# Kernel tuning notes

Measured on AMD Instinct MI355X. Metric: run time of the kernel, lower is better.

Reference implementation:

```python
import jax, jax.numpy as jnp
from jax import lax
import numpy as np

B, K, H, W = 16, 8, 256, 256


def setup_inputs() -> dict:
    key = jax.random.key(0)
    masks = jax.random.normal(key, (B, K, H, W), dtype=jnp.float32)
    return {"masks": masks}


def _nlccs_loss_one(mask):
    """Per-mask loss. mask: (H, W) float, already rescaled/clamped.

    Replicates cv2.connectedComponentsWithStats (8-connectivity, background is
    a single label regardless of connectivity), sorts components by area, and
    suppresses (zeroes a pmask over) the bounding box of the second-largest
    component, then returns mean(pmask * mask).
    """
    h, w = mask.shape
    S = h * w  # sentinel / background label
    sent = jnp.int32(S)
    fg = lax.stop_gradient(mask) > 0.5  # cv2 threshold (arr > 0.5)
    idx = jnp.arange(S, dtype=jnp.int32).reshape(h, w)
    lab0 = jnp.where(fg, idx, sent)

    def step(lab):
        # 8-connectivity neighbor-min propagation (cv2 default connectivity=8)
        p = jnp.pad(lab, 1, constant_values=S)
        m = lab
        for dy in (-1, 0, 1):
            for dx in (-1, 0, 1):
                if dy == 0 and dx == 0:
                    continue
                m = jnp.minimum(m, p[1 + dy:1 + dy + h, 1 + dx:1 + dx + w])
        lab = jnp.where(fg, m, sent)
        # pointer jumping: lab <- lab[lab] for log-time convergence
        ext = jnp.concatenate([lab.reshape(-1), jnp.array([S], jnp.int32)])
        return jnp.where(fg, ext[lab], sent)

    def cond(c):
        lab, prev = c
        return jnp.any(lab != prev)

    def body(c):
        lab, _ = c
        return step(lab), lab

    lab, _ = lax.while_loop(cond, body, (step(lab0), lab0))

    # per-label areas; background pixels all share label S (like cv2 label 0)
    areas = jnp.zeros(S + 1, jnp.int32).at[lab.reshape(-1)].add(1)
    _, top_idx = lax.top_k(areas, 2)
    second = top_idx[1]  # stats sorted by area -> stats[-2]

    # bounding box of the second-largest component
    sel = lab == second
    rows = jnp.arange(h, dtype=jnp.int32)[:, None]
    cols = jnp.arange(w, dtype=jnp.int32)[None, :]
    h0 = jnp.min(jnp.where(sel, rows, h))
    h1 = jnp.max(jnp.where(sel, rows, -1)) + 1
    w0 = jnp.min(jnp.where(sel, cols, w))
    w1 = jnp.max(jnp.where(sel, cols, -1)) + 1
    inside = (rows >= h0) & (rows < h1) & (cols >= w0) & (cols < w1)
    pmask = 1.0 - inside.astype(mask.dtype)  # pmask[h0:h1, w0:w1] = 0
    return (pmask * mask).mean()


def reference(masks):
    # masks: (b, k, h, w)
    m = jnp.maximum((masks + 1.0) * 0.5, 0.0)  # ((masks+1)/2).clamp(min=0)
    flat = m.reshape(-1, m.shape[-2], m.shape[-1])  # (b*k, h, w)
    losses = jax.vmap(_nlccs_loss_one)(flat)
    return losses.mean()
```

## Files before the change

kernel.cpp:

```cpp
#include <hip/hip_runtime.h>

#define HH 256
#define WW 256
#define SS 65536
#define NM 128
#define TRR 16
#define NT2 16
#define RMX 2048
#define SPT 1024
#define SPM 16384

struct Meta {
  double dsum[NM];
  int h0[NM]; int h1[NM]; int w0[NM]; int w1[NM];
};

__device__ __forceinline__ int find_c(int* L, int x) {
  int p = L[x];
  if (p == x) return x;
  int root = p, q = L[root];
  while (q != root) { root = q; q = L[root]; }
  if (root != p) L[x] = root;
  return root;
}

__device__ void unite(int* L, int a, int b) {
  bool done = false;
  do {
    a = find_c(L, a);
    b = find_c(L, b);
    if (a < b)      { int old = atomicMin(&L[b], a); done = (old == b); b = old; }
    else if (b < a) { int old = atomicMin(&L[a], b); done = (old == a); a = old; }
    else done = true;
  } while (!done);
}

__device__ __forceinline__ int find_halve(int* L, int x) {
  int p = L[x];
  while (p != x) {
    int gp = L[p];
    if (gp == p) return p;
    L[x] = gp;
    x = p; p = gp;
  }
  return x;
}

__device__ __forceinline__ int cid(const unsigned long long* rm,
                                   const int* rpre, int r) {
  int w = r >> 6, b = r & 63;
  return rpre[w] + (int)__popcll(rm[w] & (b ? ((1ull << b) - 1) : 0ull));
}

__device__ __forceinline__ unsigned long long mask_le(int b) {
  return (b == 63) ? ~0ull : ((1ull << (b + 1)) - 1);
}
__device__ __forceinline__ unsigned long long mask_lt(int b) {
  return b ? ((1ull << b) - 1) : 0ull;
}

__global__ __launch_bounds__(512)
void k_local(const float* __restrict__ in, int cb,
             int* __restrict__ gp, int* __restrict__ ga,
             unsigned int* __restrict__ gbb, unsigned short* __restrict__ gl,
             unsigned short* __restrict__ gbrow, int* __restrict__ gnr,
             double* __restrict__ tdsum, unsigned int* __restrict__ tbb,
             int* __restrict__ gfg0) {
  __shared__ unsigned long long sfgw[TRR][4];
  __shared__ unsigned char sfgc[TRR][32];
  __shared__ unsigned long long srs[TRR][4];
  __shared__ int wpre64[64];
  __shared__ int snr;
  __shared__ int sspan[RMX];
  __shared__ int suf[RMX];
  __shared__ unsigned long long rootm[32];
  __shared__ int rpre[32];
  __shared__ int sA[SPT], sW0[SPT], sW1[SPT], sH0[SPT], sH1[SPT];
  __shared__ double sred[8];
  __shared__ int sbb[4][8];

  int q = blockIdx.x, lm = q >> 4, tile = q & 15;
  int tid = threadIdx.x, lane = tid & 63, wv = tid >> 6;
  int gm = cb + lm, R0 = tile << 4;

  int r1 = tid >> 5, cs = tid & 31;
  const float4* src =
      (const float4*)(in + ((size_t)gm << 16) + ((R0 + r1) << 8) + (cs << 3));
  double dsum = 0.0;
  unsigned int fgb = 0;
  for (int k = 0; k < 2; k++) {
    float4 v = src[k];
    float m0 = fmaxf((v.x + 1.0f) * 0.5f, 0.0f);
    float m1 = fmaxf((v.y + 1.0f) * 0.5f, 0.0f);
    float m2 = fmaxf((v.z + 1.0f) * 0.5f, 0.0f);
    float m3 = fmaxf((v.w + 1.0f) * 0.5f, 0.0f);
    dsum += (double)m0 + (double)m1 + (double)m2 + (double)m3;
    fgb |= ((m0 > 0.5f) ? 1u : 0u) << (4 * k);
    fgb |= ((m1 > 0.5f) ? 1u : 0u) << (4 * k + 1);
    fgb |= ((m2 > 0.5f) ? 1u : 0u) << (4 * k + 2);
    fgb |= ((m3 > 0.5f) ? 1u : 0u) << (4 * k + 3);
  }
  sfgc[r1][cs] = (unsigned char)fgb;
  __syncthreads();
  if (tid < 64) {
    int row = tid >> 2, w = tid & 3;
    const unsigned char* pc = &sfgc[row][w << 3];
    unsigned long long wd = 0;
    for (int i = 0; i < 8; i++) wd |= ((unsigned long long)pc[i]) << (i << 3);
    sfgw[row][w] = wd;
  }
  __syncthreads();

  if (tid < 64) {
    int row = tid >> 2, w = tid & 3;
    unsigned long long W = sfgw[row][w];
    unsigned long long carry = (w > 0) ? (sfgw[row][w - 1] >> 63) : 0ull;
    unsigned long long rs = W & ~((W << 1) | carry);
    srs[row][w] = rs;
    int cnt = (int)__popcll(rs);
    int sa = cnt;
    for (int off = 1; off < 64; off <<= 1) {
      int t = __shfl_up(sa, off);
      if (tid >= off) sa += t;
    }
    wpre64[tid] = sa - cnt;
    if (tid == 63) snr = sa;
    int id = sa - cnt;
    unsigned long long bits = rs;
    while (bits) {
      int a = (int)__ffsll(bits) - 1;
      bits &= bits - 1;
      int A = (w << 6) + a;
      unsigned long long inv = ~(W >> a);
      int len = inv ? ((int)__ffsll(inv) - 1) : (64 - a);
      if (len == 64 - a) {
        for (int w2 = w + 1; w2 < 4; w2++) {
          unsigned long long iv2 = ~sfgw[row][w2];
          int t = iv2 ? ((int)__ffsll(iv2) - 1) : 64;
          len += t;
          if (t < 64) break;
        }
      }
      sspan[id] = (row << 16) | (A << 8) | (A + len - 1);
      suf[id] = id;
      id++;
    }
  } else {
    for (int s = tid - 64; s < SPT; s += 448) {
      sA[s] = 0; sW0[s] = WW; sW1[s] = -1; sH0[s] = TRR; sH1[s] = -1;
    }
  }
  __syncthreads();

  int nr = snr;

  for (int i = tid; i < nr; i += 512) {
    int sp = sspan[i];
    int row = sp >> 16, a = (sp >> 8) & 255, b = sp & 255;
    if (row == 0) continue;
    int lo = max(a - 1, 0), hi = min(b + 1, 255);
    const unsigned long long* Wp = sfgw[row - 1];
    const unsigned long long* Rp = srs[row - 1];
    int prebase = (row - 1) << 2;
    int lw = lo >> 6, lb = lo & 63;
    if (((Wp[lw] >> lb) & 1) && !((Rp[lw] >> lb) & 1)) {
      int j = wpre64[prebase + lw] + (int)__popcll(Rp[lw] & mask_le(lb)) - 1;
      unite(suf, i, j);
    }
    for (int w = lw; w <= (hi >> 6); w++) {
      unsigned long long m = Rp[w];
      if (w == lw) m &= ~mask_lt(lb);
      if (w == (hi >> 6)) m &= mask_le(hi & 63);
      int base2 = wpre64[prebase + w];
      while (m) {
        int bb = (int)__ffsll(m) - 1;
        m &= m - 1;
        int j = base2 + (int)__popcll(Rp[w] & mask_lt(bb));
        unite(suf, i, j);
      }
    }
  }
  __syncthreads();

  for (int j = 0; j < 4; j++) {
    int i = tid + (j << 9);
    unsigned long long bal = __ballot(i < nr && suf[i] == i);
    if (lane == 0) rootm[wv + (j << 3)] = bal;
  }
  __syncthreads();
  if (tid < 32) {
    int pc = (int)__popcll(rootm[tid]);
    int sa = pc;
    for (int off = 1; off < 32; off <<= 1) {
      int t = __shfl_up(sa, off);
      if (tid >= off) sa += t;
    }
    rpre[tid] = sa - pc;
  }
  __syncthreads();

  for (int i = tid; i < nr; i += 512) {
    int root = find_halve(suf, i);
    int id = cid(rootm, rpre, root);
    int sp = sspan[i];
    int row = sp >> 16, a = (sp >> 8) & 255, b = sp & 255;
    atomicAdd(&sA[id], b - a + 1);
    if (a < sW0[id]) atomicMin(&sW0[id], a);
    if (b > sW1[id]) atomicMax(&sW1[id], b);
    if (row < sH0[id]) atomicMin(&sH0[id], row);
    if (row > sH1[id]) atomicMax(&sH1[id], row);
  }
  __syncthreads();

  int nc = rpre[31] + (int)__popcll(rootm[31]);
  for (int i = tid; i < nr; i += 512) {
    if (suf[i] == i) {
      int id = cid(rootm, rpre, i);
      int gid = (lm << 14) + (tile << 10) + id;
      int sp = sspan[i];
      gp[gid] = gid;
      ga[gid] = sA[id];
      gl[gid] = (unsigned short)((tile << 12) + ((sp >> 16) << 8) +
                                 ((sp >> 8) & 255));
      gbb[gid] = ((unsigned)(R0 + sH0[id]) << 24) | ((unsigned)sW0[id] << 16)
               | ((unsigned)(R0 + sH1[id]) << 8) | (unsigned)sW1[id];
    }
  }
  {
    int c = tid & 255, topbot = tid >> 8;
    int brow = topbot ? (TRR - 1) : 0;
    unsigned short val = 0xFFFF;
    if ((sfgw[brow][c >> 6] >> (c & 63)) & 1) {
      int w = c >> 6, bb = c & 63;
      int id = wpre64[(brow << 2) + w] +
               (int)__popcll(srs[brow][w] & mask_le(bb)) - 1;
      int root = find_halve(suf, id);
      val = (unsigned short)((tile << 10) + cid(rootm, rpre, root));
    }
    gbrow[(q << 9) + (topbot ? 256 : 0) + c] = val;
  }
  if (tid == 0) gnr[q] = nc;

  int c = tid & 255, half = (tid >> 8) << 3;
  int bh0r = TRR, bh1r = -1;
  bool anybg = false;
  for (int row = half; row < half + 8; row++) {
    if (!((sfgw[row][c >> 6] >> (c & 63)) & 1)) {
      anybg = true;
      bh0r = min(bh0r, row); bh1r = max(bh1r, row);
    }
  }
  int bw0r = anybg ? c : WW, bw1r = anybg ? c : -1;
  for (int off = 32; off > 0; off >>= 1) {
    bw0r = min(bw0r, __shfl_down(bw0r, off));
    bw1r = max(bw1r, __shfl_down(bw1r, off));
    bh0r = min(bh0r, __shfl_down(bh0r, off));
    bh1r = max(bh1r, __shfl_down(bh1r, off));
  }
  if (lane == 0) { sbb[0][wv] = bw0r; sbb[1][wv] = bw1r;
                   sbb[2][wv] = bh0r; sbb[3][wv] = bh1r; }
  for (int off = 32; off > 0; off >>= 1) dsum += __shfl_down(dsum, off);
  if (lane == 0) sred[wv] = dsum;
  __syncthreads();
  if (tid == 0) {
    int a0 = sbb[0][0], a1 = sbb[1][0], a2 = sbb[2][0], a3 = sbb[3][0];
    for (int i = 1; i < 8; i++) {
      a0 = min(a0, sbb[0][i]); a1 = max(a1, sbb[1][i]);
      a2 = min(a2, sbb[2][i]); a3 = max(a3, sbb[3][i]);
    }
    unsigned pack = (a1 >= 0)
        ? (((unsigned)(R0 + a2) << 24) | ((unsigned)a0 << 16) |
           ((unsigned)(R0 + a3) << 8) | (unsigned)a1)
        : 0xFFFF0000u;
    tbb[q] = pack;
    double t = 0.0;
    for (int i = 0; i < 8; i++) t += sred[i];
    tdsum[q] = t;
    if (tile == 0) gfg0[lm] = (int)(sfgw[0][0] & 1ull);
  }
}

__global__ void k_seam(int* __restrict__ gp,
                       const unsigned short* __restrict__ gbrow) {
  int b = blockIdx.x;
  int lm = b / 15, s = b % 15;
  int tb = lm << 4;
  int sbase = lm << 14;
  const unsigned short* up = gbrow + ((tb + s) << 9) + 256;
  const unsigned short* lo = gbrow + ((tb + s + 1) << 9);
  int c = threadIdx.x;
  unsigned short v16 = lo[c];
  if (v16 == 0xFFFF) return;
  int v = sbase + v16;
  bool wfg = (c > 0) && (lo[c - 1] != 0xFFFF);
  unsigned short n16 = up[c];
  if (!wfg) {
    if (n16 != 0xFFFF) unite(gp, v, sbase + n16);
    else if (c > 0 && up[c - 1] != 0xFFFF) unite(gp, v, sbase + up[c - 1]);
  }
  if (n16 == 0xFFFF && c < 255 && up[c + 1] != 0xFFFF)
    unite(gp, v, sbase + up[c + 1]);
}

__global__ void k_push(int* __restrict__ gp, int* __restrict__ ga,
                       const int* __restrict__ gnr) {
  int q = blockIdx.x;
  int lm = q >> 4;
  int sbase = lm << 14;
  int nc = gnr[q];
  int tid = threadIdx.x, lane = tid & 63;
  for (int t = 0; t < 4; t++) {
    int slot = (t << 8) + tid;
    int r = -1, a = 0;
    if (slot < nc) {
      int gid = sbase + ((q & 15) << 10) + slot;
      int rr = find_c(gp, gid);
      if (rr != gid) { r = rr; a = ga[gid]; }
    }
    bool pend = (r >= 0);
    while (__any(pend)) {
      unsigned long long mk = __ballot(pend);
      int srcl = (int)__ffsll(mk) - 1;
      int lead = __shfl(r, srcl);
      bool mine = pend && (r == lead);
      int v = mine ? a : 0;
      for (int off = 32; off > 0; off >>= 1) v += __shfl_down(v, off);
      int tot = __shfl(v, 0);
      if (lane == srcl) atomicAdd(&ga[lead], tot);
      pend = pend && !mine;
    }
  }
}

__global__ __launch_bounds__(1024)
void k_mask(int* __restrict__ gp, const int* __restrict__ ga,
            const unsigned int* __restrict__ gbb,
            const unsigned short* __restrict__ gl,
            const int* __restrict__ gnr,
            const double* __restrict__ tdsum,
            const unsigned int* __restrict__ tbb,
            const int* __restrict__ gfg0,
            Meta* __restrict__ mt, int c0) {
  int lm = blockIdx.x, gm = c0 + lm;
  int tid = threadIdx.x;
  int tb = lm << 4;
  int sbase = lm << 14;
  int wv = tid >> 6, lane = tid & 63;
  __shared__ int sbg[4];
  __shared__ int snr16[16];

  if (tid >= 64 && tid < 80) snr16[tid - 64] = gnr[tb + (tid - 64)];
  if (tid < 64) {
    double d = 0.0;
    int h0 = 255, w0 = 255, h1 = 0, w1 = 0;
    if (tid < 16) {
      d = tdsum[tb + tid];
      unsigned bb = tbb[tb + tid];
      h0 = (int)(bb >> 24); w0 = (int)((bb >> 16) & 255);
      h1 = (int)((bb >> 8) & 255); w1 = (int)(bb & 255);
    }
    for (int off = 8; off > 0; off >>= 1) {
      d += __shfl_down(d, off);
      h0 = min(h0, __shfl_down(h0, off));
      w0 = min(w0, __shfl_down(w0, off));
      h1 = max(h1, __shfl_down(h1, off));
      w1 = max(w1, __shfl_down(w1, off));
    }
    if (tid == 0) {
      mt->dsum[gm] = d;
      sbg[0] = h0; sbg[1] = h1; sbg[2] = w0; sbg[3] = w1;
    }
  }
  __syncthreads();

  unsigned long long t1 = 0, t2 = 0;
  int fsum = 0;
  for (int s = tid; s < SPM; s += 1024) {
    if ((s & (SPT - 1)) >= snr16[s >> 10]) continue;
    int gid = sbase + s;
    if (gp[gid] == gid) {
      int a = ga[gid];
      int lab = gl[gid];
      fsum += a;
      unsigned long long key = ((unsigned long long)a << 37)
                             | ((unsigned long long)(SS - lab) << 20)
                             | (unsigned)s;
      if (key > t1) { t2 = t1; t1 = key; }
      else if (key > t2) t2 = key;
    }
  }
  for (int off = 32; off > 0; off >>= 1) {
    unsigned long long o1 = __shfl_down(t1, off), o2 = __shfl_down(t2, off);
    if (o1 > t1) { t2 = (t1 > o2) ? t1 : o2; t1 = o1; }
    else if (o1 > t2) t2 = o1;
    fsum += __shfl_down(fsum, off);
  }
  __shared__ unsigned long long s1[16], s2[16];
  __shared__ int sf[16];
  __shared__ int ssel, sslot;
  if (lane == 0) { s1[wv] = t1; s2[wv] = t2; sf[wv] = fsum; }
  __syncthreads();
  if (tid == 0) {
    t1 = s1[0]; t2 = s2[0]; fsum = sf[0];
    for (int i = 1; i < 16; i++) {
      unsigned long long o1 = s1[i], o2 = s2[i];
      if (o1 > t1) { t2 = (t1 > o2) ? t1 : o2; t1 = o1; }
      else if (o1 > t2) t2 = o1;
      fsum += sf[i];
    }
    unsigned long long bg = ((unsigned long long)(SS - fsum)) << 37;
    int zl = gfg0[lm] ? 1 : 0;
    unsigned long long zk = ((unsigned long long)(SS - zl)) << 20;
    if (bg > t1) { t2 = t1; t1 = bg; } else if (bg > t2) t2 = bg;
    if (zk > t1) { t2 = t1; t1 = zk; } else if (zk > t2) t2 = zk;
    if (t2 == bg) {
      ssel = 1;
      mt->h0[gm] = sbg[0]; mt->h1[gm] = sbg[1];
      mt->w0[gm] = sbg[2]; mt->w1[gm] = sbg[3];
    } else if (t2 == zk) {
      ssel = 2;
      mt->h0[gm] = 1; mt->h1[gm] = 0; mt->w0[gm] = 1; mt->w1[gm] = 0;
    } else {
      ssel = 0; sslot = (int)(t2 & 0xFFFFF);
    }
  }
  __syncthreads();

  if (ssel == 0) {
    int secgid = sbase + sslot;
    int h0l = HH, h1l = -1, w0l = WW, w1l = -1;
    for (int s = tid; s < SPM; s += 1024) {
      if ((s & (SPT - 1)) >= snr16[s >> 10]) continue;
      int i = sbase + s;
      if (find_c(gp, i) == secgid) {
        unsigned int bb = gbb[i];
        h0l = min(h0l, (int)(bb >> 24));
        w0l = min(w0l, (int)((bb >> 16) & 255));
        h1l = max(h1l, (int)((bb >> 8) & 255));
        w1l = max(w1l, (int)(bb & 255));
      }
    }
    for (int off = 32; off > 0; off >>= 1) {
      h0l = min(h0l, __shfl_down(h0l, off));
      w0l = min(w0l, __shfl_down(w0l, off));
      h1l = max(h1l, __shfl_down(h1l, off));
      w1l = max(w1l, __shfl_down(w1l, off));
    }
    __shared__ int r0[16], r1[16], r2[16], r3[16];
    if (lane == 0) { r0[wv] = h0l; r1[wv] = h1l; r2[wv] = w0l; r3[wv] = w1l; }
    __syncthreads();
    if (tid == 0) {
      for (int i = 1; i < 16; i++) {
        r0[0] = min(r0[0], r0[i]); r1[0] = max(r1[0], r1[i]);
        r2[0] = min(r2[0], r2[i]); r3[0] = max(r3[0], r3[i]);
      }
      mt->h0[gm] = r0[0]; mt->h1[gm] = r1[0];
      mt->w0[gm] = r2[0]; mt->w1[gm] = r3[0];
    }
  }
}

__global__ void k_inside(const float* __restrict__ in,
                         const Meta* __restrict__ mt,
                         double* __restrict__ dinsp, int c0) {
  int b = blockIdx.x;
  int lm = b >> 3, seg = b & 7;
  int gm = c0 + lm;
  int h0 = mt->h0[gm], h1 = mt->h1[gm], w0 = mt->w0[gm], w1 = mt->w1[gm];
  double acc = 0.0;
  if (h1 >= h0) {
    int cc = w0 + threadIdx.x;
    if (cc <= w1) {
      const float* base = in + ((size_t)gm << 16);
      for (int rr = h0 + seg; rr <= h1; rr += 8) {
        float x = base[(rr << 8) + cc];
        acc += (double)fmaxf((x + 1.0f) * 0.5f, 0.0f);
      }
    }
  }
  for (int off = 32; off > 0; off >>= 1) acc += __shfl_down(acc, off);
  __shared__ double sd[4];
  int wid = threadIdx.x >> 6, lane = threadIdx.x & 63;
  if (lane == 0) sd[wid] = acc;
  __syncthreads();
  if (threadIdx.x == 0)
    dinsp[(gm << 3) + seg] = sd[0] + sd[1] + sd[2] + sd[3];
}

__global__ void k_final(const Meta* __restrict__ mt,
                        const double* __restrict__ dinsp,
                        float* __restrict__ out) {
  __shared__ double sd[NM];
  int t = threadIdx.x;
  double di = 0.0;
  for (int s = 0; s < 8; s++) di += dinsp[(t << 3) + s];
  sd[t] = (mt->dsum[t] - di) / (double)SS;
  __syncthreads();
  for (int off = 64; off > 0; off >>= 1) {
    if (t < off) sd[t] += sd[t + off];
    __syncthreads();
  }
  if (t == 0) out[0] = (float)(sd[0] / (double)NM);
}

extern "C" void kernel_launch(void* const* d_in, const int* in_sizes, int n_in,
                              void* d_out, int out_size, void* d_ws,
                              size_t ws_size, hipStream_t stream) {
  const float* in = (const float*)d_in[0];
  float* out = (float*)d_out;

  Meta* mt = (Meta*)d_ws;
  const size_t meta_bytes = (sizeof(Meta) + 255) & ~(size_t)255;
  char* base = (char*)d_ws + meta_bytes;
  size_t fixed = (size_t)NM * 8 * sizeof(double);
  size_t avail = (ws_size > meta_bytes + fixed)
                     ? (ws_size - meta_bytes - fixed) : 0;
  const size_t per_mask = (size_t)NT2 * 8 + NT2 * 4 + 4 +
                          (size_t)SPM * (4 + 4 + 4 + 2) +
                          (size_t)NT2 * 512 * 2 + NT2 * 4;
  int chunk = (int)(avail / per_mask);
  if (chunk > NM) chunk = NM;
  if (chunk < 1) return;

  char* ptr = base;
  double* dinsp = (double*)ptr;        ptr += fixed;
  double* tdsum = (double*)ptr;        ptr += (size_t)chunk * NT2 * 8;
  int* gp = (int*)ptr;                 ptr += (size_t)chunk * SPM * 4;
  int* ga = (int*)ptr;                 ptr += (size_t)chunk * SPM * 4;
  unsigned int* gbb = (unsigned int*)ptr;       ptr += (size_t)chunk * SPM * 4;
  unsigned short* gl = (unsigned short*)ptr;    ptr += (size_t)chunk * SPM * 2;
  unsigned short* gbrow = (unsigned short*)ptr; ptr += (size_t)chunk * NT2 * 512 * 2;
  int* gnr = (int*)ptr;                ptr += (size_t)chunk * NT2 * 4;
  unsigned int* tbb = (unsigned int*)ptr;       ptr += (size_t)chunk * NT2 * 4;
  int* gfg0 = (int*)ptr;

  for (int c0 = 0; c0 < NM; c0 += chunk) {
    int cn = (chunk < NM - c0) ? chunk : (NM - c0);
    k_local<<<cn * NT2, 512, 0, stream>>>(in, c0, gp, ga, gbb, gl, gbrow,
                                          gnr, tdsum, tbb, gfg0);
    k_seam <<<cn * 15, 256, 0, stream>>>(gp, gbrow);
    k_push <<<cn * NT2, 256, 0, stream>>>(gp, ga, gnr);
    k_mask <<<cn, 1024, 0, stream>>>(gp, ga, gbb, gl, gnr, tdsum, tbb,
                                     gfg0, mt, c0);
    k_inside<<<cn * 8, 256, 0, stream>>>(in, mt, dinsp, c0);
  }
  k_final<<<1, 128, 0, stream>>>(mt, dinsp, out);
}
```

Baseline: 193.1 us.

## Split per-mask top-2 and bbox sweep into per-tile kernels

The single 1024-thread-per-mask k_mask kernel becomes three stages. A per-tile top-2/area-sum kernel runs 16 blocks per mask, a tiny 64-thread kernel merges the tile results and picks the second component, and a per-tile sweep kernel computes its bounding box with atomic min/max. This spreads the work over 16x more blocks so more CUs are busy, and loops only over each tile's used slots. It costs two extra kernel launches per chunk, additional workspace, and global atomics.

```diff
diff --git a/kernel.cpp b/kernel.cpp
--- a/kernel.cpp
+++ b/kernel.cpp
@@ -332,51 +332,21 @@
   }
 }
 
-__global__ __launch_bounds__(1024)
-void k_mask(int* __restrict__ gp, const int* __restrict__ ga,
-            const unsigned int* __restrict__ gbb,
-            const unsigned short* __restrict__ gl,
-            const int* __restrict__ gnr,
-            const double* __restrict__ tdsum,
-            const unsigned int* __restrict__ tbb,
-            const int* __restrict__ gfg0,
-            Meta* __restrict__ mt, int c0) {
-  int lm = blockIdx.x, gm = c0 + lm;
-  int tid = threadIdx.x;
-  int tb = lm << 4;
+__global__ void k_top2p(const int* __restrict__ gp, const int* __restrict__ ga,
+                        const unsigned short* __restrict__ gl,
+                        const int* __restrict__ gnr,
+                        unsigned long long* __restrict__ tt1,
+                        unsigned long long* __restrict__ tt2,
+                        int* __restrict__ tfs) {
+  int q = blockIdx.x;
+  int lm = q >> 4, tile = q & 15;
   int sbase = lm << 14;
-  int wv = tid >> 6, lane = tid & 63;
-  __shared__ int sbg[4];
-  __shared__ int snr16[16];
-
-  if (tid >= 64 && tid < 80) snr16[tid - 64] = gnr[tb + (tid - 64)];
-  if (tid < 64) {
-    double d = 0.0;
-    int h0 = 255, w0 = 255, h1 = 0, w1 = 0;
-    if (tid < 16) {
-      d = tdsum[tb + tid];
-      unsigned bb = tbb[tb + tid];
-      h0 = (int)(bb >> 24); w0 = (int)((bb >> 16) & 255);
-      h1 = (int)((bb >> 8) & 255); w1 = (int)(bb & 255);
-    }
-    for (int off = 8; off > 0; off >>= 1) {
-      d += __shfl_down(d, off);
-      h0 = min(h0, __shfl_down(h0, off));
-      w0 = min(w0, __shfl_down(w0, off));
-      h1 = max(h1, __shfl_down(h1, off));
-      w1 = max(w1, __shfl_down(w1, off));
-    }
-    if (tid == 0) {
-      mt->dsum[gm] = d;
-      sbg[0] = h0; sbg[1] = h1; sbg[2] = w0; sbg[3] = w1;
-    }
-  }
-  __syncthreads();
-
+  int nc = gnr[q];
+  int tid = threadIdx.x, lane = tid & 63, wv = tid >> 6;
   unsigned long long t1 = 0, t2 = 0;
   int fsum = 0;
-  for (int s = tid; s < SPM; s += 1024) {
-    if ((s & (SPT - 1)) >= snr16[s >> 10]) continue;
+  for (int sl = tid; sl < nc; sl += 256) {
+    int s = (tile << 10) + sl;
     int gid = sbase + s;
     if (gp[gid] == gid) {
       int a = ga[gid];
@@ -395,67 +365,116 @@
     else if (o1 > t2) t2 = o1;
     fsum += __shfl_down(fsum, off);
   }
-  __shared__ unsigned long long s1[16], s2[16];
-  __shared__ int sf[16];
-  __shared__ int ssel, sslot;
+  __shared__ unsigned long long s1[4], s2[4];
+  __shared__ int sf[4];
   if (lane == 0) { s1[wv] = t1; s2[wv] = t2; sf[wv] = fsum; }
   __syncthreads();
   if (tid == 0) {
-    t1 = s1[0]; t2 = s2[0]; fsum = sf[0];
-    for (int i = 1; i < 16; i++) {
+    for (int i = 1; i < 4; i++) {
       unsigned long long o1 = s1[i], o2 = s2[i];
       if (o1 > t1) { t2 = (t1 > o2) ? t1 : o2; t1 = o1; }
       else if (o1 > t2) t2 = o1;
       fsum += sf[i];
     }
+    tt1[q] = t1; tt2[q] = t2; tfs[q] = fsum;
+  }
+}
+
+__global__ __launch_bounds__(64)
+void k_mask(const double* __restrict__ tdsum,
+            const unsigned int* __restrict__ tbb,
+            const unsigned long long* __restrict__ tt1,
+            const unsigned long long* __restrict__ tt2,
+            const int* __restrict__ tfs, const int* __restrict__ gfg0,
+            int* __restrict__ psec, Meta* __restrict__ mt, int c0) {
+  int lm = blockIdx.x, gm = c0 + lm;
+  int tid = threadIdx.x;
+  int tb = lm << 4;
+  double d = 0.0;
+  int h0 = 255, w0 = 255, h1 = 0, w1 = 0;
+  unsigned long long t1 = 0, t2 = 0;
+  int fsum = 0;
+  if (tid < 16) {
+    d = tdsum[tb + tid];
+    unsigned bb = tbb[tb + tid];
+    h0 = (int)(bb >> 24); w0 = (int)((bb >> 16) & 255);
+    h1 = (int)((bb >> 8) & 255); w1 = (int)(bb & 255);
+    t1 = tt1[tb + tid]; t2 = tt2[tb + tid]; fsum = tfs[tb + tid];
+  }
+  for (int off = 8; off > 0; off >>= 1) {
+    d += __shfl_down(d, off);
+    h0 = min(h0, __shfl_down(h0, off));
+    w0 = min(w0, __shfl_down(w0, off));
+    h1 = max(h1, __shfl_down(h1, off));
+    w1 = max(w1, __shfl_down(w1, off));
+    unsigned long long o1 = __shfl_down(t1, off), o2 = __shfl_down(t2, off);
+    if (o1 > t1) { t2 = (t1 > o2) ? t1 : o2; t1 = o1; }
+    else if (o1 > t2) t2 = o1;
+    fsum += __shfl_down(fsum, off);
+  }
+  if (tid == 0) {
+    mt->dsum[gm] = d;
     unsigned long long bg = ((unsigned long long)(SS - fsum)) << 37;
     int zl = gfg0[lm] ? 1 : 0;
     unsigned long long zk = ((unsigned long long)(SS - zl)) << 20;
     if (bg > t1) { t2 = t1; t1 = bg; } else if (bg > t2) t2 = bg;
     if (zk > t1) { t2 = t1; t1 = zk; } else if (zk > t2) t2 = zk;
     if (t2 == bg) {
-      ssel = 1;
-      mt->h0[gm] = sbg[0]; mt->h1[gm] = sbg[1];
-      mt->w0[gm] = sbg[2]; mt->w1[gm] = sbg[3];
+      psec[lm] = -1;
+      mt->h0[gm] = h0; mt->h1[gm] = h1; mt->w0[gm] = w0; mt->w1[gm] = w1;
     } else if (t2 == zk) {
-      ssel = 2;
+      psec[lm] = -1;
       mt->h0[gm] = 1; mt->h1[gm] = 0; mt->w0[gm] = 1; mt->w1[gm] = 0;
     } else {
-      ssel = 0; sslot = (int)(t2 & 0xFFFFF);
-    }
-  }
-  __syncthreads();
-
-  if (ssel == 0) {
-    int secgid = sbase + sslot;
-    int h0l = HH, h1l = -1, w0l = WW, w1l = -1;
-    for (int s = tid; s < SPM; s += 1024) {
-      if ((s & (SPT - 1)) >= snr16[s >> 10]) continue;
-      int i = sbase + s;
-      if (find_c(gp, i) == secgid) {
-        unsigned int bb = gbb[i];
-        h0l = min(h0l, (int)(bb >> 24));
-        w0l = min(w0l, (int)((bb >> 16) & 255));
-        h1l = max(h1l, (int)((bb >> 8) & 255));
-        w1l = max(w1l, (int)(bb & 255));
-      }
-    }
-    for (int off = 32; off > 0; off >>= 1) {
-      h0l = min(h0l, __shfl_down(h0l, off));
-      w0l = min(w0l, __shfl_down(w0l, off));
-      h1l = max(h1l, __shfl_down(h1l, off));
-      w1l = max(w1l, __shfl_down(w1l, off));
-    }
-    __shared__ int r0[16], r1[16], r2[16], r3[16];
-    if (lane == 0) { r0[wv] = h0l; r1[wv] = h1l; r2[wv] = w0l; r3[wv] = w1l; }
-    __syncthreads();
-    if (tid == 0) {
-      for (int i = 1; i < 16; i++) {
-        r0[0] = min(r0[0], r0[i]); r1[0] = max(r1[0], r1[i]);
-        r2[0] = min(r2[0], r2[i]); r3[0] = max(r3[0], r3[i]);
-      }
-      mt->h0[gm] = r0[0]; mt->h1[gm] = r1[0];
-      mt->w0[gm] = r2[0]; mt->w1[gm] = r3[0];
+      psec[lm] = (lm << 14) + (int)(t2 & 0xFFFFF);
+      mt->h0[gm] = HH; mt->h1[gm] = -1; mt->w0[gm] = WW; mt->w1[gm] = -1;
+    }
+  }
+}
+
+__global__ void k_sweep(int* __restrict__ gp,
+                        const unsigned int* __restrict__ gbb,
+                        const int* __restrict__ gnr,
+                        const int* __restrict__ psec,
+                        Meta* __restrict__ mt, int c0) {
+  int q = blockIdx.x;
+  int lm = q >> 4, tile = q & 15;
+  int gm = c0 + lm;
+  int sec = psec[lm];
+  if (sec < 0) return;
+  int sbase = lm << 14;
+  int nc = gnr[q];
+  int tid = threadIdx.x, lane = tid & 63, wv = tid >> 6;
+  int h0l = HH, h1l = -1, w0l = WW, w1l = -1;
+  for (int sl = tid; sl < nc; sl += 256) {
+    int gid = sbase + (tile << 10) + sl;
+    if (find_c(gp, gid) == sec) {
+      unsigned int bb = gbb[gid];
+      h0l = min(h0l, (int)(bb >> 24));
+      w0l = min(w0l, (int)((bb >> 16) & 255));
+      h1l = max(h1l, (int)((bb >> 8) & 255));
+      w1l = max(w1l, (int)(bb & 255));
+    }
+  }
+  for (int off = 32; off > 0; off >>= 1) {
+    h0l = min(h0l, __shfl_down(h0l, off));
+    w0l = min(w0l, __shfl_down(w0l, off));
+    h1l = max(h1l, __shfl_down(h1l, off));
+    w1l = max(w1l, __shfl_down(w1l, off));
+  }
+  __shared__ int r0[4], r1[4], r2[4], r3[4];
+  if (lane == 0) { r0[wv] = h0l; r1[wv] = h1l; r2[wv] = w0l; r3[wv] = w1l; }
+  __syncthreads();
+  if (tid == 0) {
+    for (int i = 1; i < 4; i++) {
+      r0[0] = min(r0[0], r0[i]); r1[0] = max(r1[0], r1[i]);
+      r2[0] = min(r2[0], r2[i]); r3[0] = max(r3[0], r3[i]);
+    }
+    if (r1[0] >= 0) {
+      atomicMin(&mt->h0[gm], r0[0]);
+      atomicMax(&mt->h1[gm], r1[0]);
+      atomicMin(&mt->w0[gm], r2[0]);
+      atomicMax(&mt->w1[gm], r3[0]);
     }
   }
 }
@@ -517,7 +536,8 @@
                      ? (ws_size - meta_bytes - fixed) : 0;
   const size_t per_mask = (size_t)NT2 * 8 + NT2 * 4 + 4 +
                           (size_t)SPM * (4 + 4 + 4 + 2) +
-                          (size_t)NT2 * 512 * 2 + NT2 * 4;
+                          (size_t)NT2 * 512 * 2 + NT2 * 4 +
+                          (size_t)NT2 * (8 + 8 + 4) + 4;
   int chunk = (int)(avail / per_mask);
   if (chunk > NM) chunk = NM;
   if (chunk < 1) return;
@@ -525,6 +545,10 @@
   char* ptr = base;
   double* dinsp = (double*)ptr;        ptr += fixed;
   double* tdsum = (double*)ptr;        ptr += (size_t)chunk * NT2 * 8;
+  unsigned long long* tt1 = (unsigned long long*)ptr;
+  ptr += (size_t)chunk * NT2 * 8;
+  unsigned long long* tt2 = (unsigned long long*)ptr;
+  ptr += (size_t)chunk * NT2 * 8;
   int* gp = (int*)ptr;                 ptr += (size_t)chunk * SPM * 4;
   int* ga = (int*)ptr;                 ptr += (size_t)chunk * SPM * 4;
   unsigned int* gbb = (unsigned int*)ptr;       ptr += (size_t)chunk * SPM * 4;
@@ -532,7 +556,9 @@
   unsigned short* gbrow = (unsigned short*)ptr; ptr += (size_t)chunk * NT2 * 512 * 2;
   int* gnr = (int*)ptr;                ptr += (size_t)chunk * NT2 * 4;
   unsigned int* tbb = (unsigned int*)ptr;       ptr += (size_t)chunk * NT2 * 4;
-  int* gfg0 = (int*)ptr;
+  int* tfs = (int*)ptr;                ptr += (size_t)chunk * NT2 * 4;
+  int* gfg0 = (int*)ptr;               ptr += (size_t)chunk * 4;
+  int* psec = (int*)ptr;
 
   for (int c0 = 0; c0 < NM; c0 += chunk) {
     int cn = (chunk < NM - c0) ? chunk : (NM - c0);
@@ -540,8 +566,10 @@
                                           gnr, tdsum, tbb, gfg0);
     k_seam <<<cn * 15, 256, 0, stream>>>(gp, gbrow);
     k_push <<<cn * NT2, 256, 0, stream>>>(gp, ga, gnr);
-    k_mask <<<cn, 1024, 0, stream>>>(gp, ga, gbb, gl, gnr, tdsum, tbb,
-                                     gfg0, mt, c0);
+    k_top2p<<<cn * NT2, 256, 0, stream>>>(gp, ga, gl, gnr, tt1, tt2, tfs);
+    k_mask <<<cn, 64, 0, stream>>>(tdsum, tbb, tt1, tt2, tfs, gfg0, psec,
+                                   mt, c0);
+    k_sweep<<<cn * NT2, 256, 0, stream>>>(gp, gbb, gnr, psec, mt, c0);
     k_inside<<<cn * 8, 256, 0, stream>>>(in, mt, dinsp, c0);
   }
   k_final<<<1, 128, 0, stream>>>(mt, dinsp, out);
```

New measurement: 188.1 us. 2.6% less time.
